# Kernel optimization log

Hardware: AMD Instinct MI355X
Metric: run time of the kernel (lower is better)

## Reference

```python
import jax, jax.numpy as jnp
import numpy as np

N = 50000        # nodes
E = 800000       # edges
D = 128          # node_dim
H = 128          # hidden_dim
R = 64           # num_rbf
L = 4            # num_layers
G = 64           # graphs in batch
CUTOFF = 6.0
GAMMA = 10.0


def setup_inputs() -> dict:
    key = jax.random.key(0)
    ks = jax.random.split(key, 16)
    s = 0.05

    def p(k, shape):
        return jax.random.normal(k, shape, jnp.float32) * s

    x = jax.random.normal(ks[0], (N, D), jnp.float32)
    pos = jax.random.normal(ks[1], (N, 3), jnp.float32)
    edge_index = jax.random.randint(ks[2], (2, E), 0, N)
    batch = jnp.sort(jax.random.randint(ks[3], (N,), 0, G))

    return {
        "x": x, "pos": pos, "edge_index": edge_index, "batch": batch,
        # per-layer stacked params (leading dim L)
        "W_node": p(ks[4], (L, D, H)), "b_node": jnp.zeros((L, H), jnp.float32),
        "W_rbf": p(ks[5], (L, R, H)), "b_rbf": jnp.zeros((L, H), jnp.float32),
        "W_e1": p(ks[6], (L, 3 * H, H)), "b_e1": jnp.zeros((L, H), jnp.float32),
        "W_e2": p(ks[7], (L, H, H)), "b_e2": jnp.zeros((L, H), jnp.float32),
        "W_u1": p(ks[8], (L, H, H)), "b_u1": jnp.zeros((L, H), jnp.float32),
        "W_u2": p(ks[9], (L, H, D)), "b_u2": jnp.zeros((L, D), jnp.float32),
        # final readout MLP
        "W_f1": p(ks[10], (D, H)), "b_f1": jnp.zeros((H,), jnp.float32),
        "W_f2": p(ks[11], (H, 1)), "b_f2": jnp.zeros((1,), jnp.float32),
    }


def reference(x, pos, edge_index, batch,
              W_node, b_node, W_rbf, b_rbf,
              W_e1, b_e1, W_e2, b_e2,
              W_u1, b_u1, W_u2, b_u2,
              W_f1, b_f1, W_f2, b_f2):
    row, col = edge_index[0], edge_index[1]   # row = source (j), col = target (i)
    silu = jax.nn.silu

    # RBF expansion of edge distances (pos is constant across layers, compute once)
    centers = jnp.linspace(0.0, CUTOFF, R).astype(x.dtype)
    dist = jnp.linalg.norm(pos[row] - pos[col], axis=-1)            # [E]
    rbf = jnp.exp(-GAMMA * (dist[:, None] - centers) ** 2)          # [E, R]

    for l in range(L):
        h = x @ W_node[l] + b_node[l]                               # [N, H]
        e = rbf @ W_rbf[l] + b_rbf[l]                               # [E, H]
        # message: cat([x_i, x_j, edge_attr]) -> MLP
        msg = jnp.concatenate([h[col], h[row], e], axis=-1)         # [E, 3H]
        m = silu(msg @ W_e1[l] + b_e1[l]) @ W_e2[l] + b_e2[l]       # [E, H]
        agg = jax.ops.segment_sum(m, col, num_segments=N)           # [N, H]
        x = silu(agg @ W_u1[l] + b_u1[l]) @ W_u2[l] + b_u2[l]       # [N, D]

    g = jax.ops.segment_sum(x, batch, num_segments=G)               # [G, D]
    out = silu(g @ W_f1 + b_f1) @ W_f2 + b_f2                       # [G, 1]
    return out.reshape(-1)
```

## Files before the change

kernel.cpp:

```cpp
#include <hip/hip_runtime.h>
#include <hip/hip_bf16.h>

#define NN 50000
#define NE 800000
#define DD 128
#define HH 128
#define RR 64
#define LL 4
#define GG 64
#define EB 64

typedef float f4 __attribute__((ext_vector_type(4)));
typedef __attribute__((ext_vector_type(8))) short bf16x8;
typedef __attribute__((ext_vector_type(4))) float f32x4;

__device__ __forceinline__ float silu1(float v)
{
    return v * __builtin_amdgcn_rcpf(1.0f + __expf(-v));
}

__device__ __forceinline__ unsigned short f2bf(float f)
{
    union { float f; unsigned u; } x; x.f = f;
    unsigned r = x.u + 0x7fffu + ((x.u >> 16) & 1u);
    return (unsigned short)(r >> 16);
}
__device__ __forceinline__ float bf2f(unsigned short h)
{
    union { unsigned u; float f; } x; x.u = ((unsigned)h) << 16; return x.f;
}
__device__ __forceinline__ unsigned pk2bf(float a, float b)
{
    __hip_bfloat162 h = __float22bfloat162_rn(float2{a, b});
    union { __hip_bfloat162 h; unsigned u; } c; c.h = h;
    return c.u;
}

__global__ void fillz_kernel(float* __restrict__ p, int n4)
{
    int i = blockIdx.x * 256 + threadIdx.x;
    if (i < n4) ((f4*)p)[i] = (f4){0.f, 0.f, 0.f, 0.f};
}

__global__ void hist_kernel(const int* __restrict__ ecol, int* __restrict__ cnt)
{
    int e = blockIdx.x * 256 + threadIdx.x;
    if (e < NE) atomicAdd(&cnt[ecol[e]], 1);
}

__global__ void scan_kernel(const int* __restrict__ cnt, int* __restrict__ cur)
{
    __shared__ int s[1024];
    int t = threadIdx.x;
    const int CH = 49;
    int a0 = t * CH, a1 = a0 + CH; if (a1 > NN) a1 = NN; if (a0 > NN) a0 = NN;
    int s0 = 0;
    for (int i = a0; i < a1; ++i) s0 += cnt[i];
    s[t] = s0;
    __syncthreads();
    for (int off = 1; off < 1024; off <<= 1) {
        int v = (t >= off) ? s[t - off] : 0;
        __syncthreads();
        s[t] += v;
        __syncthreads();
    }
    int base = (t == 0) ? 0 : s[t - 1];
    for (int i = a0; i < a1; ++i) { cur[i] = base; base += cnt[i]; }
}

__global__ void scatter_kernel(const float* __restrict__ pos,
                               const int* __restrict__ erow, const int* __restrict__ ecol,
                               int* __restrict__ cur,
                               int* __restrict__ srow, int* __restrict__ scol,
                               float* __restrict__ sdist)
{
    int e = blockIdx.x * 256 + threadIdx.x;
    if (e >= NE) return;
    int r = erow[e], c = ecol[e];
    int p = atomicAdd(&cur[c], 1);
    srow[p] = r;
    scol[p] = c;
    float dx = pos[r * 3 + 0] - pos[c * 3 + 0];
    float dy = pos[r * 3 + 1] - pos[c * 3 + 1];
    float dz = pos[r * 3 + 2] - pos[c * 3 + 2];
    sdist[p] = sqrtf(dx * dx + dy * dy + dz * dz);
}

__global__ void gstart_kernel(const int* __restrict__ batch, int* __restrict__ gstart)
{
    int i = blockIdx.x * 256 + threadIdx.x;
    if (i >= NN) return;
    int b = batch[i];
    if (i == 0) {
        for (int g = 0; g <= b; ++g) gstart[g] = 0;
    } else {
        int bp = batch[i - 1];
        for (int g = bp + 1; g <= b; ++g) gstart[g] = i;
    }
    if (i == NN - 1) {
        for (int g = b + 1; g <= GG; ++g) gstart[g] = NN;
    }
}

__global__ void fold_kernel(const float* __restrict__ Wnode, const float* __restrict__ Wrbf,
                            const float* __restrict__ We1,
                            const float* __restrict__ bnode, const float* __restrict__ brbf,
                            const float* __restrict__ be1,
                            float* __restrict__ Wpa, float* __restrict__ Wqb,
                            float* __restrict__ Wc, float* __restrict__ bmsg)
{
    int l = blockIdx.y;
    int o = blockIdx.x * 256 + threadIdx.x;
    const float* We1l = We1 + (size_t)l * 384 * 128;
    if (o < 16384) {
        int r = o >> 7, c = o & 127;
        const float* A = Wnode + (size_t)l * 16384;
        float s = 0.f;
        for (int k = 0; k < 128; ++k) s += A[r * 128 + k] * We1l[k * 128 + c];
        Wpa[(size_t)l * 16384 + o] = s;
    } else if (o < 32768) {
        int oo = o - 16384;
        int r = oo >> 7, c = oo & 127;
        const float* A = Wnode + (size_t)l * 16384;
        const float* B = We1l + 16384;
        float s = 0.f;
        for (int k = 0; k < 128; ++k) s += A[r * 128 + k] * B[k * 128 + c];
        Wqb[(size_t)l * 16384 + oo] = s;
    } else if (o < 40960) {
        int oo = o - 32768;
        int r = oo >> 7, c = oo & 127;
        const float* A = Wrbf + (size_t)l * 8192;
        const float* B = We1l + 32768;
        float s = 0.f;
        for (int k = 0; k < 128; ++k) s += A[r * 128 + k] * B[k * 128 + c];
        Wc[(size_t)l * 8192 + oo] = s;
    } else if (o < 41088) {
        int j = o - 40960;
        float s = be1[l * 128 + j];
        for (int k = 0; k < 128; ++k) {
            float w = We1l[k * 128 + j] + We1l[(128 + k) * 128 + j];
            s += bnode[l * 128 + k] * w + brbf[l * 128 + k] * We1l[(256 + k) * 128 + j];
        }
        bmsg[l * 128 + j] = s;
    }
}

__global__ void pack_kernel(const float* __restrict__ M, unsigned short* __restrict__ pk, int K)
{
    int idx = blockIdx.x * 256 + threadIdx.x;
    if (idx >= K * 128) return;
    int k = idx >> 7, c = idx & 127;
    int kc = k >> 5, hi = (k >> 3) & 3, j = k & 7;
    int cbG = c >> 4, lo = c & 15;
    int lane = hi * 16 + lo;
    pk[(((kc * 8 + cbG) * 64 + lane) * 8) + j] = f2bf(M[idx]);
}

__global__ void pack2_kernel(const float* __restrict__ M,
                             unsigned short* __restrict__ pkh,
                             unsigned short* __restrict__ pkl, int K)
{
    int idx = blockIdx.x * 256 + threadIdx.x;
    if (idx >= K * 128) return;
    int k = idx >> 7, c = idx & 127;
    int kc = k >> 5, hi = (k >> 3) & 3, j = k & 7;
    int cbG = c >> 4, lo = c & 15;
    int lane = hi * 16 + lo;
    int o = (((kc * 8 + cbG) * 64 + lane) * 8) + j;
    float v = M[idx];
    unsigned short h = f2bf(v);
    pkh[o] = h;
    pkl[o] = f2bf(v - bf2f(h));
}

__global__ __launch_bounds__(256, 2)
void nodepq_kernel(const float* __restrict__ X,
                   const unsigned short* __restrict__ pkpah,
                   const unsigned short* __restrict__ pkpal,
                   const unsigned short* __restrict__ pkqbh,
                   const unsigned short* __restrict__ pkqbl,
                   float* __restrict__ P, float* __restrict__ Q,
                   float* __restrict__ agg)
{
    __shared__ unsigned short s_h[64 * 128];
    __shared__ unsigned short s_l[64 * 128];

    const int tid = threadIdx.x;
    const int w = tid >> 6;
    const int lane = tid & 63;
    const int lo = lane & 15, hi = lane >> 4;
    const int r0 = blockIdx.x * 64;
    const int colbase = w * 32;

    for (int i = tid; i < 1024; i += 256) {
        int e = i >> 4, cg = i & 15;
        int r = r0 + e;
        union { unsigned short u16[8]; f4 v; } H, L;
        if (r < NN) {
            f4 v0 = ((const f4*)X)[(size_t)r * 32 + cg * 2];
            f4 v1 = ((const f4*)X)[(size_t)r * 32 + cg * 2 + 1];
#pragma unroll
            for (int q = 0; q < 4; ++q) {
                unsigned short h0 = f2bf(v0[q]);
                unsigned short h1 = f2bf(v1[q]);
                H.u16[q] = h0;     L.u16[q] = f2bf(v0[q] - bf2f(h0));
                H.u16[4 + q] = h1; L.u16[4 + q] = f2bf(v1[q] - bf2f(h1));
            }
        } else {
#pragma unroll
            for (int q = 0; q < 8; ++q) { H.u16[q] = 0; L.u16[q] = 0; }
        }
        int byte = e * 256 + ((cg * 16) ^ ((e & 7) << 4));
        *reinterpret_cast<f4*>((char*)s_h + byte) = H.v;
        *reinterpret_cast<f4*>((char*)s_l + byte) = L.v;
    }
    for (int i = tid; i < 2048; i += 256) {
        int e = i >> 5, cc = i & 31;
        int r = r0 + e;
        if (r < NN) ((f4*)agg)[(size_t)r * 32 + cc] = (f4){0.f, 0.f, 0.f, 0.f};
    }
    __syncthreads();

    f32x4 accp[4][2], accq[4][2];
#pragma unroll
    for (int rb = 0; rb < 4; ++rb)
#pragma unroll
        for (int cb = 0; cb < 2; ++cb) {
            accp[rb][cb] = (f32x4){0.f, 0.f, 0.f, 0.f};
            accq[rb][cb] = (f32x4){0.f, 0.f, 0.f, 0.f};
        }

#pragma unroll
    for (int kc = 0; kc < 4; ++kc) {
        bf16x8 ah[4], al[4];
#pragma unroll
        for (int rb = 0; rb < 4; ++rb) {
            int row = rb * 16 + lo;
            int byte = row * 256 + ((kc * 64 + hi * 16) ^ ((row & 7) << 4));
            ah[rb] = *reinterpret_cast<const bf16x8*>((const char*)s_h + byte);
            al[rb] = *reinterpret_cast<const bf16x8*>((const char*)s_l + byte);
        }
#pragma unroll
        for (int cb = 0; cb < 2; ++cb) {
            size_t boff = ((size_t)((kc * 8 + w * 2 + cb) * 64 + lane)) * 8;
            bf16x8 bph = *reinterpret_cast<const bf16x8*>(pkpah + boff);
            bf16x8 bpl = *reinterpret_cast<const bf16x8*>(pkpal + boff);
            bf16x8 bqh = *reinterpret_cast<const bf16x8*>(pkqbh + boff);
            bf16x8 bql = *reinterpret_cast<const bf16x8*>(pkqbl + boff);
#pragma unroll
            for (int rb = 0; rb < 4; ++rb) {
                accp[rb][cb] = __builtin_amdgcn_mfma_f32_16x16x32_bf16(ah[rb], bph, accp[rb][cb], 0, 0, 0);
                accp[rb][cb] = __builtin_amdgcn_mfma_f32_16x16x32_bf16(al[rb], bph, accp[rb][cb], 0, 0, 0);
                accp[rb][cb] = __builtin_amdgcn_mfma_f32_16x16x32_bf16(ah[rb], bpl, accp[rb][cb], 0, 0, 0);
                accq[rb][cb] = __builtin_amdgcn_mfma_f32_16x16x32_bf16(ah[rb], bqh, accq[rb][cb], 0, 0, 0);
                accq[rb][cb] = __builtin_amdgcn_mfma_f32_16x16x32_bf16(al[rb], bqh, accq[rb][cb], 0, 0, 0);
                accq[rb][cb] = __builtin_amdgcn_mfma_f32_16x16x32_bf16(ah[rb], bql, accq[rb][cb], 0, 0, 0);
            }
        }
    }

#pragma unroll
    for (int rb = 0; rb < 4; ++rb)
#pragma unroll
        for (int r = 0; r < 4; ++r) {
            int row = r0 + rb * 16 + hi * 4 + r;
            if (row < NN) {
#pragma unroll
                for (int cb = 0; cb < 2; ++cb) {
                    int col = colbase + cb * 16 + lo;
                    P[(size_t)row * 128 + col] = accp[rb][cb][r];
                    Q[(size_t)row * 128 + col] = accq[rb][cb][r];
                }
            }
        }
}

__global__ __launch_bounds__(256, 4)
void edge_mfma_kernel(const float* __restrict__ P, const float* __restrict__ Q,
                      const float* __restrict__ sdist,
                      const int* __restrict__ srow, const int* __restrict__ scol,
                      const unsigned short* __restrict__ pk1,
                      const unsigned short* __restrict__ pk3,
                      const float* __restrict__ bmsg, const float* __restrict__ be2,
                      float* __restrict__ agg)
{
    __shared__ unsigned short s_t[EB * 128];
    __shared__ float s_d[EB];
    __shared__ int s_row[EB], s_col[EB];
    __shared__ int s_rs[EB + 1];
    __shared__ int s_nr;

    const int tid = threadIdx.x;
    const int w = tid >> 6;
    const int lane = tid & 63;
    const int lo = lane & 15, hi = lane >> 4;
    const int e0 = blockIdx.x * EB;
    const int ew = w * 16;

    if (tid < EB) {
        s_d[tid] = sdist[e0 + tid];
        s_row[tid] = srow[e0 + tid];
        s_col[tid] = scol[e0 + tid];
    }
    __syncthreads();

    if (w == 0) {
        int c = s_col[lane];
        bool flag = (lane == 0) || (c != s_col[lane - 1]);
        unsigned long long m = __ballot(flag);
        if (flag) {
            int rank = __popcll(m & ((1ull << lane) - 1ull));
            s_rs[rank] = lane;
        }
        if (lane == 0) {
            int nr = __popcll(m);
            s_nr = nr;
            s_rs[nr] = EB;
        }
    }

    f32x4 acc[8];
#pragma unroll
    for (int cb = 0; cb < 8; ++cb) acc[cb] = (f32x4){0.f, 0.f, 0.f, 0.f};

    const float dvv = s_d[ew + lo];
    const float step = 6.0f / 63.0f;
#pragma unroll
    for (int kc = 0; kc < 2; ++kc) {
        union { bf16x8 v; unsigned u32[4]; } U;
#pragma unroll
        for (int j2 = 0; j2 < 4; ++j2) {
            float t0 = dvv - (float)(kc * 32 + hi * 8 + 2 * j2) * step;
            float t1 = dvv - (float)(kc * 32 + hi * 8 + 2 * j2 + 1) * step;
            U.u32[j2] = pk2bf(__expf(-10.0f * t0 * t0), __expf(-10.0f * t1 * t1));
        }
#pragma unroll
        for (int cb = 0; cb < 8; ++cb) {
            bf16x8 b = *reinterpret_cast<const bf16x8*>(
                pk1 + ((size_t)((kc * 8 + cb) * 64 + lane)) * 8);
            acc[cb] = __builtin_amdgcn_mfma_f32_16x16x32_bf16(U.v, b, acc[cb], 0, 0, 0);
        }
    }

#pragma unroll
    for (int r = 0; r < 4; ++r) {
        int e = ew + hi * 4 + r;
        int sw = (e & 7) << 4;
#pragma unroll
        for (int cb = 0; cb < 8; cb += 2) {
            unsigned pk = pk2bf(acc[cb][r], acc[cb + 1][r]);
            int c0 = cb * 16 + lo, c1 = c0 + 16;
            *(unsigned short*)((char*)s_t + e * 256 + ((c0 * 2) ^ sw)) = (unsigned short)pk;
            *(unsigned short*)((char*)s_t + e * 256 + ((c1 * 2) ^ sw)) = (unsigned short)(pk >> 16);
        }
    }
    __syncthreads();

    {
        const int f4c = tid & 31;
        const int ebase = (tid >> 5) * 8;
        f4 bmv = ((const f4*)bmsg)[f4c];
#pragma unroll
        for (int p = 0; p < 8; ++p) {
            int e = ebase + p;
            int nc = s_col[e], nr = s_row[e];
            f4 pv = ((const f4*)(P + (size_t)nc * 128))[f4c];
            f4 qv = ((const f4*)(Q + (size_t)nr * 128))[f4c];
            int byte = e * 256 + ((f4c * 8) ^ ((e & 7) << 4));
            unsigned long long c1 = *(unsigned long long*)((char*)s_t + byte);
            float t[4];
#pragma unroll
            for (int j = 0; j < 4; ++j) {
                float c1f = bf2f((unsigned short)(c1 >> (16 * j)));
                t[j] = silu1(c1f + pv[j] + qv[j] + bmv[j]);
            }
            unsigned lo32 = pk2bf(t[0], t[1]);
            unsigned hi32 = pk2bf(t[2], t[3]);
            *(unsigned long long*)((char*)s_t + byte) =
                (unsigned long long)lo32 | ((unsigned long long)hi32 << 32);
        }
    }
    __syncthreads();

    f32x4 acc2[8];
#pragma unroll
    for (int cb = 0; cb < 8; ++cb) acc2[cb] = (f32x4){0.f, 0.f, 0.f, 0.f};

    {
        const int rowA = ew + lo;
        const int swA = (rowA & 7) << 4;
#pragma unroll
        for (int kc = 0; kc < 4; ++kc) {
            bf16x8 a = *reinterpret_cast<const bf16x8*>(
                (const char*)s_t + rowA * 256 + ((kc * 64 + hi * 16) ^ swA));
#pragma unroll
            for (int cb = 0; cb < 8; ++cb) {
                bf16x8 b = *reinterpret_cast<const bf16x8*>(
                    pk3 + ((size_t)((kc * 8 + cb) * 64 + lane)) * 8);
                acc2[cb] = __builtin_amdgcn_mfma_f32_16x16x32_bf16(a, b, acc2[cb], 0, 0, 0);
            }
        }
    }

    float be2c[8];
#pragma unroll
    for (int cb = 0; cb < 8; ++cb) be2c[cb] = be2[cb * 16 + lo];

    int nruns = s_nr;
    for (int ri = 0; ri < nruns; ++ri) {
        int a0 = s_rs[ri], b0 = s_rs[ri + 1];
        if (b0 <= ew || a0 >= ew + 16) continue;
        int la = a0 - ew; if (la < 0) la = 0;
        int lb = b0 - ew; if (lb > 16) lb = 16;
        int node = s_col[a0];
        float s[8];
#pragma unroll
        for (int cb = 0; cb < 8; ++cb) s[cb] = 0.f;
#pragma unroll
        for (int r = 0; r < 4; ++r) {
            int el = hi * 4 + r;
            bool in = (el >= la) && (el < lb);
#pragma unroll
            for (int cb = 0; cb < 8; ++cb)
                s[cb] += in ? acc2[cb][r] : 0.f;
        }
#pragma unroll
        for (int cb = 0; cb < 8; ++cb) {
            s[cb] += __shfl_xor(s[cb], 16, 64);
            s[cb] += __shfl_xor(s[cb], 32, 64);
        }
        if (hi == 0) {
            float len = (float)(lb - la);
            float* dst = agg + (size_t)node * 128;
#pragma unroll
            for (int cb = 0; cb < 8; ++cb)
                atomicAdd(dst + cb * 16 + lo, s[cb] + len * be2c[cb]);
        }
    }
}

__global__ __launch_bounds__(256, 2)
void nodeupd_kernel(const float* __restrict__ AGG,
                    const unsigned short* __restrict__ pku1h,
                    const unsigned short* __restrict__ pku1l,
                    const float* __restrict__ bu1,
                    const unsigned short* __restrict__ pku2h,
                    const unsigned short* __restrict__ pku2l,
                    const float* __restrict__ bu2,
                    float* __restrict__ Xout)
{
    __shared__ unsigned short s_h[64 * 128];
    __shared__ unsigned short s_l[64 * 128];

    const int tid = threadIdx.x;
    const int w = tid >> 6;
    const int lane = tid & 63;
    const int lo = lane & 15, hi = lane >> 4;
    const int r0 = blockIdx.x * 64;
    const int colbase = w * 32;

    for (int i = tid; i < 1024; i += 256) {
        int e = i >> 4, cg = i & 15;
        int r = r0 + e;
        union { unsigned short u16[8]; f4 v; } H, L;
        if (r < NN) {
            f4 v0 = ((const f4*)AGG)[(size_t)r * 32 + cg * 2];
            f4 v1 = ((const f4*)AGG)[(size_t)r * 32 + cg * 2 + 1];
#pragma unroll
            for (int q = 0; q < 4; ++q) {
                unsigned short h0 = f2bf(v0[q]);
                unsigned short h1 = f2bf(v1[q]);
                H.u16[q] = h0;     L.u16[q] = f2bf(v0[q] - bf2f(h0));
                H.u16[4 + q] = h1; L.u16[4 + q] = f2bf(v1[q] - bf2f(h1));
            }
        } else {
#pragma unroll
            for (int q = 0; q < 8; ++q) { H.u16[q] = 0; L.u16[q] = 0; }
        }
        int byte = e * 256 + ((cg * 16) ^ ((e & 7) << 4));
        *reinterpret_cast<f4*>((char*)s_h + byte) = H.v;
        *reinterpret_cast<f4*>((char*)s_l + byte) = L.v;
    }
    __syncthreads();

    f32x4 acc[4][2];
#pragma unroll
    for (int rb = 0; rb < 4; ++rb)
#pragma unroll
        for (int cb = 0; cb < 2; ++cb) acc[rb][cb] = (f32x4){0.f, 0.f, 0.f, 0.f};

#pragma unroll
    for (int kc = 0; kc < 4; ++kc) {
        bf16x8 ah[4], al[4];
#pragma unroll
        for (int rb = 0; rb < 4; ++rb) {
            int row = rb * 16 + lo;
            int byte = row * 256 + ((kc * 64 + hi * 16) ^ ((row & 7) << 4));
            ah[rb] = *reinterpret_cast<const bf16x8*>((const char*)s_h + byte);
            al[rb] = *reinterpret_cast<const bf16x8*>((const char*)s_l + byte);
        }
#pragma unroll
        for (int cb = 0; cb < 2; ++cb) {
            size_t boff = ((size_t)((kc * 8 + w * 2 + cb) * 64 + lane)) * 8;
            bf16x8 bh = *reinterpret_cast<const bf16x8*>(pku1h + boff);
            bf16x8 bl = *reinterpret_cast<const bf16x8*>(pku1l + boff);
#pragma unroll
            for (int rb = 0; rb < 4; ++rb) {
                acc[rb][cb] = __builtin_amdgcn_mfma_f32_16x16x32_bf16(ah[rb], bh, acc[rb][cb], 0, 0, 0);
                acc[rb][cb] = __builtin_amdgcn_mfma_f32_16x16x32_bf16(al[rb], bh, acc[rb][cb], 0, 0, 0);
                acc[rb][cb] = __builtin_amdgcn_mfma_f32_16x16x32_bf16(ah[rb], bl, acc[rb][cb], 0, 0, 0);
            }
        }
    }

    float b1c[2];
#pragma unroll
    for (int cb = 0; cb < 2; ++cb) b1c[cb] = bu1[colbase + cb * 16 + lo];

    __syncthreads();

#pragma unroll
    for (int rb = 0; rb < 4; ++rb)
#pragma unroll
        for (int r = 0; r < 4; ++r) {
            int row = rb * 16 + hi * 4 + r;
#pragma unroll
            for (int cb = 0; cb < 2; ++cb) {
                int col = colbase + cb * 16 + lo;
                float t = silu1(acc[rb][cb][r] + b1c[cb]);
                unsigned short th = f2bf(t);
                unsigned short tl = f2bf(t - bf2f(th));
                int byte = row * 256 + ((col * 2) ^ ((row & 7) << 4));
                *(unsigned short*)((char*)s_h + byte) = th;
                *(unsigned short*)((char*)s_l + byte) = tl;
            }
        }
    __syncthreads();

    f32x4 acc2[4][2];
#pragma unroll
    for (int rb = 0; rb < 4; ++rb)
#pragma unroll
        for (int cb = 0; cb < 2; ++cb) acc2[rb][cb] = (f32x4){0.f, 0.f, 0.f, 0.f};

#pragma unroll
    for (int kc = 0; kc < 4; ++kc) {
        bf16x8 ah[4], al[4];
#pragma unroll
        for (int rb = 0; rb < 4; ++rb) {
            int row = rb * 16 + lo;
            int byte = row * 256 + ((kc * 64 + hi * 16) ^ ((row & 7) << 4));
            ah[rb] = *reinterpret_cast<const bf16x8*>((const char*)s_h + byte);
            al[rb] = *reinterpret_cast<const bf16x8*>((const char*)s_l + byte);
        }
#pragma unroll
        for (int cb = 0; cb < 2; ++cb) {
            size_t boff = ((size_t)((kc * 8 + w * 2 + cb) * 64 + lane)) * 8;
            bf16x8 bh = *reinterpret_cast<const bf16x8*>(pku2h + boff);
            bf16x8 bl = *reinterpret_cast<const bf16x8*>(pku2l + boff);
#pragma unroll
            for (int rb = 0; rb < 4; ++rb) {
                acc2[rb][cb] = __builtin_amdgcn_mfma_f32_16x16x32_bf16(ah[rb], bh, acc2[rb][cb], 0, 0, 0);
                acc2[rb][cb] = __builtin_amdgcn_mfma_f32_16x16x32_bf16(al[rb], bh, acc2[rb][cb], 0, 0, 0);
                acc2[rb][cb] = __builtin_amdgcn_mfma_f32_16x16x32_bf16(ah[rb], bl, acc2[rb][cb], 0, 0, 0);
            }
        }
    }

    float b2c[2];
#pragma unroll
    for (int cb = 0; cb < 2; ++cb) b2c[cb] = bu2[colbase + cb * 16 + lo];

#pragma unroll
    for (int rb = 0; rb < 4; ++rb)
#pragma unroll
        for (int r = 0; r < 4; ++r) {
            int row = r0 + rb * 16 + hi * 4 + r;
            if (row < NN) {
#pragma unroll
                for (int cb = 0; cb < 2; ++cb) {
                    int col = colbase + cb * 16 + lo;
                    Xout[(size_t)row * 128 + col] = acc2[rb][cb][r] + b2c[cb];
                }
            }
        }
}

__global__ void gsum2_kernel(const float* __restrict__ X, const int* __restrict__ gstart,
                             float* __restrict__ Gm)
{
    __shared__ f4 red[32][8];
    int g = blockIdx.x;
    int q = blockIdx.y;
    int cq = threadIdx.x & 7;
    int cf = q * 8 + cq;
    int rg = threadIdx.x >> 3;
    int i0 = gstart[g], i1 = gstart[g + 1];
    f4 s = {0.f, 0.f, 0.f, 0.f};
    for (int i = i0 + rg; i < i1; i += 32)
        s += ((const f4*)X)[(size_t)i * 32 + cf];
    red[rg][cq] = s;
    __syncthreads();
    for (int off = 16; off >= 1; off >>= 1) {
        if (rg < off) red[rg][cq] += red[rg + off][cq];
        __syncthreads();
    }
    if (rg == 0) ((f4*)Gm)[g * 32 + cf] = red[0][cq];
}

__global__ void final_kernel(const float* __restrict__ Gm,
                             const float* __restrict__ Wf1, const float* __restrict__ bf1,
                             const float* __restrict__ Wf2, const float* __restrict__ bf2,
                             float* __restrict__ out)
{
    __shared__ float red[128];
    int g = blockIdx.x;
    int j = threadIdx.x;
    float s = bf1[j];
    for (int k = 0; k < 128; ++k) s += Gm[(size_t)g * 128 + k] * Wf1[k * 128 + j];
    s = silu1(s);
    red[j] = s * Wf2[j];
    __syncthreads();
    for (int off = 64; off > 0; off >>= 1) {
        if (j < off) red[j] += red[j + off];
        __syncthreads();
    }
    if (j == 0) out[g] = red[0] + bf2[0];
}

extern "C" void kernel_launch(void* const* d_in, const int* in_sizes, int n_in,
                              void* d_out, int out_size, void* d_ws, size_t ws_size,
                              hipStream_t stream)
{
    const float* x     = (const float*)d_in[0];
    const float* pos   = (const float*)d_in[1];
    const int*   eidx  = (const int*)d_in[2];
    const int*   batch = (const int*)d_in[3];
    const float* Wnode = (const float*)d_in[4];
    const float* bnode = (const float*)d_in[5];
    const float* Wrbf  = (const float*)d_in[6];
    const float* brbf  = (const float*)d_in[7];
    const float* We1   = (const float*)d_in[8];
    const float* be1   = (const float*)d_in[9];
    const float* We2   = (const float*)d_in[10];
    const float* be2   = (const float*)d_in[11];
    const float* Wu1   = (const float*)d_in[12];
    const float* bu1   = (const float*)d_in[13];
    const float* Wu2   = (const float*)d_in[14];
    const float* bu2   = (const float*)d_in[15];
    const float* Wf1   = (const float*)d_in[16];
    const float* bf1   = (const float*)d_in[17];
    const float* Wf2   = (const float*)d_in[18];
    const float* bf2   = (const float*)d_in[19];

    const int* erow = eidx;
    const int* ecol = eidx + NE;

    char* wsb = (char*)d_ws;
    size_t off = 0;
    auto take = [&](size_t bytes) -> char* {
        char* p = wsb + off;
        off += (bytes + 255) & ~(size_t)255;
        return p;
    };
    float* Pb    = (float*)take((size_t)NN * HH * 4);
    float* Qb    = (float*)take((size_t)NN * HH * 4);
    float* aggb  = (float*)take((size_t)NN * HH * 4);
    float* xa    = (float*)take((size_t)NN * DD * 4);
    float* gm    = (float*)take((size_t)GG * DD * 4);
    float* Wpa   = (float*)take((size_t)LL * DD * HH * 4);
    float* Wqb   = (float*)take((size_t)LL * DD * HH * 4);
    float* Wcc   = (float*)take((size_t)LL * RR * HH * 4);
    float* bmsg  = (float*)take((size_t)LL * HH * 4);
    int*   cnt   = (int*)take((size_t)NN * 4);
    int*   cur   = (int*)take((size_t)NN * 4);
    int*   srow  = (int*)take((size_t)NE * 4);
    int*   scol  = (int*)take((size_t)NE * 4);
    float* sdist = (float*)take((size_t)NE * 4);
    int*   gst   = (int*)take((size_t)(GG + 1) * 4);
    unsigned short* pk1   = (unsigned short*)take((size_t)LL * RR * HH * 2);
    unsigned short* pk3   = (unsigned short*)take((size_t)LL * HH * HH * 2);
    unsigned short* pkpah = (unsigned short*)take((size_t)LL * DD * HH * 2);
    unsigned short* pkpal = (unsigned short*)take((size_t)LL * DD * HH * 2);
    unsigned short* pkqbh = (unsigned short*)take((size_t)LL * DD * HH * 2);
    unsigned short* pkqbl = (unsigned short*)take((size_t)LL * DD * HH * 2);
    unsigned short* pku1h = (unsigned short*)take((size_t)LL * HH * HH * 2);
    unsigned short* pku1l = (unsigned short*)take((size_t)LL * HH * HH * 2);
    unsigned short* pku2h = (unsigned short*)take((size_t)LL * HH * DD * 2);
    unsigned short* pku2l = (unsigned short*)take((size_t)LL * HH * DD * 2);

    if (off > ws_size) return;

    fillz_kernel<<<(NN + 1023) / 1024, 256, 0, stream>>>((float*)cnt, NN / 4);
    hist_kernel<<<(NE + 255) / 256, 256, 0, stream>>>(ecol, cnt);
    scan_kernel<<<1, 1024, 0, stream>>>(cnt, cur);
    scatter_kernel<<<(NE + 255) / 256, 256, 0, stream>>>(pos, erow, ecol, cur, srow, scol, sdist);
    gstart_kernel<<<(NN + 255) / 256, 256, 0, stream>>>(batch, gst);

    dim3 foldgrid((41088 + 255) / 256, LL);
    fold_kernel<<<foldgrid, 256, 0, stream>>>(Wnode, Wrbf, We1, bnode, brbf, be1,
                                              Wpa, Wqb, Wcc, bmsg);
    for (int l = 0; l < LL; ++l) {
        pack_kernel<<<(RR * HH + 255) / 256, 256, 0, stream>>>(
            Wcc + (size_t)l * RR * HH, pk1 + (size_t)l * RR * HH, RR);
        pack_kernel<<<(HH * HH + 255) / 256, 256, 0, stream>>>(
            We2 + (size_t)l * HH * HH, pk3 + (size_t)l * HH * HH, HH);
        pack2_kernel<<<(DD * HH + 255) / 256, 256, 0, stream>>>(
            Wpa + (size_t)l * DD * HH, pkpah + (size_t)l * DD * HH,
            pkpal + (size_t)l * DD * HH, DD);
        pack2_kernel<<<(DD * HH + 255) / 256, 256, 0, stream>>>(
            Wqb + (size_t)l * DD * HH, pkqbh + (size_t)l * DD * HH,
            pkqbl + (size_t)l * DD * HH, DD);
        pack2_kernel<<<(HH * HH + 255) / 256, 256, 0, stream>>>(
            Wu1 + (size_t)l * HH * HH, pku1h + (size_t)l * HH * HH,
            pku1l + (size_t)l * HH * HH, HH);
        pack2_kernel<<<(HH * DD + 255) / 256, 256, 0, stream>>>(
            Wu2 + (size_t)l * HH * DD, pku2h + (size_t)l * HH * DD,
            pku2l + (size_t)l * HH * DD, HH);
    }

    const int nblk = (NN + 63) / 64;
    const float* xin = x;
    for (int l = 0; l < LL; ++l) {
        nodepq_kernel<<<nblk, 256, 0, stream>>>(xin,
                                                pkpah + (size_t)l * DD * HH,
                                                pkpal + (size_t)l * DD * HH,
                                                pkqbh + (size_t)l * DD * HH,
                                                pkqbl + (size_t)l * DD * HH,
                                                Pb, Qb, aggb);
        edge_mfma_kernel<<<NE / EB, 256, 0, stream>>>(Pb, Qb, sdist, srow, scol,
                                                      pk1 + (size_t)l * RR * HH,
                                                      pk3 + (size_t)l * HH * HH,
                                                      bmsg + (size_t)l * HH,
                                                      be2 + (size_t)l * HH, aggb);
        nodeupd_kernel<<<nblk, 256, 0, stream>>>(aggb,
                                                 pku1h + (size_t)l * HH * HH,
                                                 pku1l + (size_t)l * HH * HH,
                                                 bu1 + (size_t)l * HH,
                                                 pku2h + (size_t)l * HH * DD,
                                                 pku2l + (size_t)l * HH * DD,
                                                 bu2 + (size_t)l * DD, xa);
        xin = xa;
    }

    dim3 gsgrid(GG, 4);
    gsum2_kernel<<<gsgrid, 256, 0, stream>>>(xin, gst, gm);
    final_kernel<<<GG, 128, 0, stream>>>(gm, Wf1, bf1, Wf2, bf2, (float*)d_out);
}
```

Measured before the change: 923.5 us.

## Fuse node update with next layer's P/Q projection into one kernel

Adds a nodefuse kernel that runs the two-layer update MLP on the aggregated features. It keeps the new node features in shared memory as split bf16 hi/lo and immediately computes the next layer's P and Q projections. It also zeroes the aggregation buffer for the next layer. This removes the round trip of the node feature matrix through global memory and one launch per intermediate layer. The trade-off is a longer kernel with more live accumulators, which may add register pressure.

After: 914.8 us. No clear change (-0.9%).

```diff
diff --git a/kernel.cpp b/kernel.cpp
--- a/kernel.cpp
+++ b/kernel.cpp
@@ -173,6 +173,7 @@
     pkl[o] = f2bf(v - bf2f(h));
 }
 
+
 __global__ __launch_bounds__(256, 2)
 void nodepq_kernel(const float* __restrict__ X,
                    const unsigned short* __restrict__ pkpah,
@@ -437,6 +438,223 @@
                 atomicAdd(dst + cb * 16 + lo, s[cb] + len * be2c[cb]);
         }
     }
+}
+
+__global__ __launch_bounds__(256, 2)
+void nodefuse_kernel(const float* __restrict__ AGG,
+                     const unsigned short* __restrict__ pku1h,
+                     const unsigned short* __restrict__ pku1l,
+                     const float* __restrict__ bu1,
+                     const unsigned short* __restrict__ pku2h,
+                     const unsigned short* __restrict__ pku2l,
+                     const float* __restrict__ bu2,
+                     const unsigned short* __restrict__ pkpah,
+                     const unsigned short* __restrict__ pkpal,
+                     const unsigned short* __restrict__ pkqbh,
+                     const unsigned short* __restrict__ pkqbl,
+                     float* __restrict__ P, float* __restrict__ Q,
+                     float* __restrict__ agg)
+{
+    __shared__ unsigned short s_h[64 * 128];
+    __shared__ unsigned short s_l[64 * 128];
+
+    const int tid = threadIdx.x;
+    const int w = tid >> 6;
+    const int lane = tid & 63;
+    const int lo = lane & 15, hi = lane >> 4;
+    const int r0 = blockIdx.x * 64;
+    const int colbase = w * 32;
+
+    for (int i = tid; i < 1024; i += 256) {
+        int e = i >> 4, cg = i & 15;
+        int r = r0 + e;
+        union { unsigned short u16[8]; f4 v; } H, L;
+        if (r < NN) {
+            f4 v0 = ((const f4*)AGG)[(size_t)r * 32 + cg * 2];
+            f4 v1 = ((const f4*)AGG)[(size_t)r * 32 + cg * 2 + 1];
+#pragma unroll
+            for (int q = 0; q < 4; ++q) {
+                unsigned short h0 = f2bf(v0[q]);
+                unsigned short h1 = f2bf(v1[q]);
+                H.u16[q] = h0;     L.u16[q] = f2bf(v0[q] - bf2f(h0));
+                H.u16[4 + q] = h1; L.u16[4 + q] = f2bf(v1[q] - bf2f(h1));
+            }
+        } else {
+#pragma unroll
+            for (int q = 0; q < 8; ++q) { H.u16[q] = 0; L.u16[q] = 0; }
+        }
+        int byte = e * 256 + ((cg * 16) ^ ((e & 7) << 4));
+        *reinterpret_cast<f4*>((char*)s_h + byte) = H.v;
+        *reinterpret_cast<f4*>((char*)s_l + byte) = L.v;
+    }
+    __syncthreads();
+
+    for (int i = tid; i < 2048; i += 256) {
+        int e = i >> 5, cc = i & 31;
+        int r = r0 + e;
+        if (r < NN) ((f4*)agg)[(size_t)r * 32 + cc] = (f4){0.f, 0.f, 0.f, 0.f};
+    }
+
+    f32x4 acc[4][2];
+#pragma unroll
+    for (int rb = 0; rb < 4; ++rb)
+#pragma unroll
+        for (int cb = 0; cb < 2; ++cb) acc[rb][cb] = (f32x4){0.f, 0.f, 0.f, 0.f};
+
+#pragma unroll
+    for (int kc = 0; kc < 4; ++kc) {
+        bf16x8 ah[4], al[4];
+#pragma unroll
+        for (int rb = 0; rb < 4; ++rb) {
+            int row = rb * 16 + lo;
+            int byte = row * 256 + ((kc * 64 + hi * 16) ^ ((row & 7) << 4));
+            ah[rb] = *reinterpret_cast<const bf16x8*>((const char*)s_h + byte);
+            al[rb] = *reinterpret_cast<const bf16x8*>((const char*)s_l + byte);
+        }
+#pragma unroll
+        for (int cb = 0; cb < 2; ++cb) {
+            size_t boff = ((size_t)((kc * 8 + w * 2 + cb) * 64 + lane)) * 8;
+            bf16x8 bh = *reinterpret_cast<const bf16x8*>(pku1h + boff);
+            bf16x8 bl = *reinterpret_cast<const bf16x8*>(pku1l + boff);
+#pragma unroll
+            for (int rb = 0; rb < 4; ++rb) {
+                acc[rb][cb] = __builtin_amdgcn_mfma_f32_16x16x32_bf16(ah[rb], bh, acc[rb][cb], 0, 0, 0);
+                acc[rb][cb] = __builtin_amdgcn_mfma_f32_16x16x32_bf16(al[rb], bh, acc[rb][cb], 0, 0, 0);
+                acc[rb][cb] = __builtin_amdgcn_mfma_f32_16x16x32_bf16(ah[rb], bl, acc[rb][cb], 0, 0, 0);
+            }
+        }
+    }
+
+    float b1c[2];
+#pragma unroll
+    for (int cb = 0; cb < 2; ++cb) b1c[cb] = bu1[colbase + cb * 16 + lo];
+
+    __syncthreads();
+
+#pragma unroll
+    for (int rb = 0; rb < 4; ++rb)
+#pragma unroll
+        for (int r = 0; r < 4; ++r) {
+            int row = rb * 16 + hi * 4 + r;
+#pragma unroll
+            for (int cb = 0; cb < 2; ++cb) {
+                int col = colbase + cb * 16 + lo;
+                float t = silu1(acc[rb][cb][r] + b1c[cb]);
+                unsigned short th = f2bf(t);
+                unsigned short tl = f2bf(t - bf2f(th));
+                int byte = row * 256 + ((col * 2) ^ ((row & 7) << 4));
+                *(unsigned short*)((char*)s_h + byte) = th;
+                *(unsigned short*)((char*)s_l + byte) = tl;
+            }
+        }
+    __syncthreads();
+
+    f32x4 acc2[4][2];
+#pragma unroll
+    for (int rb = 0; rb < 4; ++rb)
+#pragma unroll
+        for (int cb = 0; cb < 2; ++cb) acc2[rb][cb] = (f32x4){0.f, 0.f, 0.f, 0.f};
+
+#pragma unroll
+    for (int kc = 0; kc < 4; ++kc) {
+        bf16x8 ah[4], al[4];
+#pragma unroll
+        for (int rb = 0; rb < 4; ++rb) {
+            int row = rb * 16 + lo;
+            int byte = row * 256 + ((kc * 64 + hi * 16) ^ ((row & 7) << 4));
+            ah[rb] = *reinterpret_cast<const bf16x8*>((const char*)s_h + byte);
+            al[rb] = *reinterpret_cast<const bf16x8*>((const char*)s_l + byte);
+        }
+#pragma unroll
+        for (int cb = 0; cb < 2; ++cb) {
+            size_t boff = ((size_t)((kc * 8 + w * 2 + cb) * 64 + lane)) * 8;
+            bf16x8 bh = *reinterpret_cast<const bf16x8*>(pku2h + boff);
+            bf16x8 bl = *reinterpret_cast<const bf16x8*>(pku2l + boff);
+#pragma unroll
+            for (int rb = 0; rb < 4; ++rb) {
+                acc2[rb][cb] = __builtin_amdgcn_mfma_f32_16x16x32_bf16(ah[rb], bh, acc2[rb][cb], 0, 0, 0);
+                acc2[rb][cb] = __builtin_amdgcn_mfma_f32_16x16x32_bf16(al[rb], bh, acc2[rb][cb], 0, 0, 0);
+                acc2[rb][cb] = __builtin_amdgcn_mfma_f32_16x16x32_bf16(ah[rb], bl, acc2[rb][cb], 0, 0, 0);
+            }
+        }
+    }
+
+    float b2c[2];
+#pragma unroll
+    for (int cb = 0; cb < 2; ++cb) b2c[cb] = bu2[colbase + cb * 16 + lo];
+
+    __syncthreads();
+
+#pragma unroll
+    for (int rb = 0; rb < 4; ++rb)
+#pragma unroll
+        for (int r = 0; r < 4; ++r) {
+            int row = rb * 16 + hi * 4 + r;
+#pragma unroll
+            for (int cb = 0; cb < 2; ++cb) {
+                int col = colbase + cb * 16 + lo;
+                float xv = acc2[rb][cb][r] + b2c[cb];
+                unsigned short th = f2bf(xv);
+                unsigned short tl = f2bf(xv - bf2f(th));
+                int byte = row * 256 + ((col * 2) ^ ((row & 7) << 4));
+                *(unsigned short*)((char*)s_h + byte) = th;
+                *(unsigned short*)((char*)s_l + byte) = tl;
+            }
+        }
+    __syncthreads();
+
+    f32x4 accp[4][2], accq[4][2];
+#pragma unroll
+    for (int rb = 0; rb < 4; ++rb)
+#pragma unroll
+        for (int cb = 0; cb < 2; ++cb) {
+            accp[rb][cb] = (f32x4){0.f, 0.f, 0.f, 0.f};
+            accq[rb][cb] = (f32x4){0.f, 0.f, 0.f, 0.f};
+        }
+
+#pragma unroll
+    for (int kc = 0; kc < 4; ++kc) {
+        bf16x8 ah[4], al[4];
+#pragma unroll
+        for (int rb = 0; rb < 4; ++rb) {
+            int row = rb * 16 + lo;
+            int byte = row * 256 + ((kc * 64 + hi * 16) ^ ((row & 7) << 4));
+            ah[rb] = *reinterpret_cast<const bf16x8*>((const char*)s_h + byte);
+            al[rb] = *reinterpret_cast<const bf16x8*>((const char*)s_l + byte);
+        }
+#pragma unroll
+        for (int cb = 0; cb < 2; ++cb) {
+            size_t boff = ((size_t)((kc * 8 + w * 2 + cb) * 64 + lane)) * 8;
+            bf16x8 bph = *reinterpret_cast<const bf16x8*>(pkpah + boff);
+            bf16x8 bpl = *reinterpret_cast<const bf16x8*>(pkpal + boff);
+            bf16x8 bqh = *reinterpret_cast<const bf16x8*>(pkqbh + boff);
+            bf16x8 bql = *reinterpret_cast<const bf16x8*>(pkqbl + boff);
+#pragma unroll
+            for (int rb = 0; rb < 4; ++rb) {
+                accp[rb][cb] = __builtin_amdgcn_mfma_f32_16x16x32_bf16(ah[rb], bph, accp[rb][cb], 0, 0, 0);
+                accp[rb][cb] = __builtin_amdgcn_mfma_f32_16x16x32_bf16(al[rb], bph, accp[rb][cb], 0, 0, 0);
+                accp[rb][cb] = __builtin_amdgcn_mfma_f32_16x16x32_bf16(ah[rb], bpl, accp[rb][cb], 0, 0, 0);
+                accq[rb][cb] = __builtin_amdgcn_mfma_f32_16x16x32_bf16(ah[rb], bqh, accq[rb][cb], 0, 0, 0);
+                accq[rb][cb] = __builtin_amdgcn_mfma_f32_16x16x32_bf16(al[rb], bqh, accq[rb][cb], 0, 0, 0);
+                accq[rb][cb] = __builtin_amdgcn_mfma_f32_16x16x32_bf16(ah[rb], bql, accq[rb][cb], 0, 0, 0);
+            }
+        }
+    }
+
+#pragma unroll
+    for (int rb = 0; rb < 4; ++rb)
+#pragma unroll
+        for (int r = 0; r < 4; ++r) {
+            int row = r0 + rb * 16 + hi * 4 + r;
+            if (row < NN) {
+#pragma unroll
+                for (int cb = 0; cb < 2; ++cb) {
+                    int col = colbase + cb * 16 + lo;
+                    P[(size_t)row * 128 + col] = accp[rb][cb][r];
+                    Q[(size_t)row * 128 + col] = accq[rb][cb][r];
+                }
+            }
+        }
 }
 
 __global__ __launch_bounds__(256, 2)
@@ -720,30 +938,35 @@
     }
 
     const int nblk = (NN + 63) / 64;
-    const float* xin = x;
+    nodepq_kernel<<<nblk, 256, 0, stream>>>(x, pkpah, pkpal, pkqbh, pkqbl,
+                                            Pb, Qb, aggb);
     for (int l = 0; l < LL; ++l) {
-        nodepq_kernel<<<nblk, 256, 0, stream>>>(xin,
-                                                pkpah + (size_t)l * DD * HH,
-                                                pkpal + (size_t)l * DD * HH,
-                                                pkqbh + (size_t)l * DD * HH,
-                                                pkqbl + (size_t)l * DD * HH,
-                                                Pb, Qb, aggb);
         edge_mfma_kernel<<<NE / EB, 256, 0, stream>>>(Pb, Qb, sdist, srow, scol,
                                                       pk1 + (size_t)l * RR * HH,
                                                       pk3 + (size_t)l * HH * HH,
                                                       bmsg + (size_t)l * HH,
                                                       be2 + (size_t)l * HH, aggb);
-        nodeupd_kernel<<<nblk, 256, 0, stream>>>(aggb,
-                                                 pku1h + (size_t)l * HH * HH,
-                                                 pku1l + (size_t)l * HH * HH,
-                                                 bu1 + (size_t)l * HH,
-                                                 pku2h + (size_t)l * HH * DD,
-                                                 pku2l + (size_t)l * HH * DD,
-                                                 bu2 + (size_t)l * DD, xa);
-        xin = xa;
+        if (l < LL - 1) {
+            nodefuse_kernel<<<nblk, 256, 0, stream>>>(
+                aggb,
+                pku1h + (size_t)l * HH * HH, pku1l + (size_t)l * HH * HH,
+                bu1 + (size_t)l * HH,
+                pku2h + (size_t)l * HH * DD, pku2l + (size_t)l * HH * DD,
+                bu2 + (size_t)l * DD,
+                pkpah + (size_t)(l + 1) * DD * HH, pkpal + (size_t)(l + 1) * DD * HH,
+                pkqbh + (size_t)(l + 1) * DD * HH, pkqbl + (size_t)(l + 1) * DD * HH,
+                Pb, Qb, aggb);
+        } else {
+            nodeupd_kernel<<<nblk, 256, 0, stream>>>(
+                aggb,
+                pku1h + (size_t)l * HH * HH, pku1l + (size_t)l * HH * HH,
+                bu1 + (size_t)l * HH,
+                pku2h + (size_t)l * HH * DD, pku2l + (size_t)l * HH * DD,
+                bu2 + (size_t)l * DD, xa);
+        }
     }
 
     dim3 gsgrid(GG, 4);
-    gsum2_kernel<<<gsgrid, 256, 0, stream>>>(xin, gst, gm);
+    gsum2_kernel<<<gsgrid, 256, 0, stream>>>(xa, gst, gm);
     final_kernel<<<GG, 128, 0, stream>>>(gm, Wf1, bf1, Wf2, bf2, (float*)d_out);
 }
```
